# Kernel tuning notes

Measured on AMD Instinct MI355X. Metric: run time of the kernel, lower is better.

## Reference

```python
import jax, jax.numpy as jnp
import numpy as np

NUM_NODES = 20000
SEQ_LEN = 128
IN_FEATS = 2
HIDDEN = 32
N_TOTAL = NUM_NODES * SEQ_LEN  # flattened graph size
N_EDGES = 2_000_000


def setup_inputs() -> dict:
    key = jax.random.key(0)
    ks = jax.random.split(key, 10)
    x = jax.random.normal(ks[0], (NUM_NODES, SEQ_LEN, IN_FEATS), dtype=jnp.float32)
    edge_index = jax.random.randint(ks[1], (2, N_EDGES), 0, N_TOTAL, dtype=jnp.int64)
    s = 0.1
    gcn_W = jax.random.normal(ks[2], (IN_FEATS, HIDDEN), dtype=jnp.float32) * s
    gcn_b = jnp.zeros((HIDDEN,), dtype=jnp.float32)
    w_ih = jax.random.normal(ks[3], (4 * HIDDEN, HIDDEN), dtype=jnp.float32) * s
    w_hh = jax.random.normal(ks[4], (4 * HIDDEN, HIDDEN), dtype=jnp.float32) * s
    b_ih = jax.random.normal(ks[5], (4 * HIDDEN,), dtype=jnp.float32) * s
    b_hh = jax.random.normal(ks[6], (4 * HIDDEN,), dtype=jnp.float32) * s
    fc_W = jax.random.normal(ks[7], (HIDDEN, 1), dtype=jnp.float32) * s
    fc_b = jnp.zeros((1,), dtype=jnp.float32)
    return {"x": x, "edge_index": edge_index, "gcn_W": gcn_W, "gcn_b": gcn_b,
            "w_ih": w_ih, "w_hh": w_hh, "b_ih": b_ih, "b_hh": b_hh,
            "fc_W": fc_W, "fc_b": fc_b}


def _gcn(x_flat, edge_index, W, b):
    # PyG GCNConv: add self-loops, symmetric normalization, then linear+bias.
    src, dst = edge_index[0], edge_index[1]
    n = x_flat.shape[0]
    # degree at target side, including the self-loop (+1)
    deg = jax.ops.segment_sum(jnp.ones_like(dst, dtype=x_flat.dtype), dst, num_segments=n) + 1.0
    dinv = jax.lax.rsqrt(deg)  # deg >= 1 always (self-loop)
    h = x_flat @ W  # [n, HIDDEN] transform before propagate
    norm = dinv[src] * dinv[dst]  # [E]
    msg = h[src] * norm[:, None]  # gather + per-edge scale
    agg = jax.ops.segment_sum(msg, dst, num_segments=n)
    # self-loop contribution: dinv_i * dinv_i * h_i = h_i / deg_i
    out = agg + h * (1.0 / deg)[:, None]
    return out + b


def _lstm(xs, w_ih, w_hh, b_ih, b_hh):
    # torch LSTM gate order: i, f, g, o. xs: [N, S, H] -> final hidden [N, H]
    n, s, hdim = xs.shape
    xs_t = jnp.swapaxes(xs, 0, 1)  # [S, N, H]
    # precompute input projections once (dense GEMM)
    x_proj = xs_t @ w_ih.T + b_ih + b_hh  # [S, N, 4H]

    def step(carry, xp):
        h, c = carry
        g = xp + h @ w_hh.T  # [N, 4H]
        i, f, gg, o = jnp.split(g, 4, axis=-1)
        c = jax.nn.sigmoid(f) * c + jax.nn.sigmoid(i) * jnp.tanh(gg)
        h = jax.nn.sigmoid(o) * jnp.tanh(c)
        return (h, c), None

    h0 = jnp.zeros((n, hdim), dtype=xs.dtype)
    (hn, _), _ = jax.lax.scan(step, (h0, h0), x_proj)
    return hn


def reference(x, edge_index, gcn_W, gcn_b, w_ih, w_hh, b_ih, b_hh, fc_W, fc_b):
    num_nodes, seq_len, num_feats = x.shape
    x_in = x.reshape(-1, num_feats)  # [N*S, F]
    x_gcn = jax.nn.relu(_gcn(x_in, edge_index, gcn_W, gcn_b))
    x_lstm = x_gcn.reshape(num_nodes, seq_len, -1)
    hn = _lstm(x_lstm, w_ih, w_hh, b_ih, b_hh)
    return hn @ fc_W + fc_b  # [num_nodes, 1]
```

## Files before the change

### kernel.cpp

```cpp
#include <hip/hip_runtime.h>

#define SEQ 128
#define HID 32
#define TPB 128
#define XS 56

typedef __attribute__((ext_vector_type(8))) short short8;
typedef __attribute__((ext_vector_type(4))) short short4v;
typedef __attribute__((ext_vector_type(4))) float floatx4;


__global__ void count_kernel(const int* __restrict__ idx, int E, int* __restrict__ cnt) {
    int e = (blockIdx.x * blockDim.x + threadIdx.x) * 4;
    if (((E & 3) == 0) && e + 3 < E) {
        int4 d = *(const int4*)(idx + E + e);
        atomicAdd(&cnt[d.x], 1);
        atomicAdd(&cnt[d.y], 1);
        atomicAdd(&cnt[d.z], 1);
        atomicAdd(&cnt[d.w], 1);
    } else {
        int lim = min(e + 4, E);
        for (int k = e; k < lim; ++k) atomicAdd(&cnt[idx[E + k]], 1);
    }
}

__global__ void dinv_xs_pk_kernel(const int* __restrict__ deg, float* __restrict__ dinv,
                                  const float2* __restrict__ x2, float2* __restrict__ xs2,
                                  int n) {
    int i = blockIdx.x * blockDim.x + threadIdx.x;
    if (i < n) {
        float dv = rsqrtf((float)deg[i] + 1.0f);
        dinv[i] = dv;
        float2 xx = x2[i];
        xs2[i] = make_float2(xx.x * dv, xx.y * dv);
    }
}

__global__ void dinv_kernel(float* __restrict__ buf, int n) {
    int i = blockIdx.x * blockDim.x + threadIdx.x;
    if (i < n) buf[i] = rsqrtf((float)__float_as_int(buf[i]) + 1.0f);
}

__device__ __forceinline__ unsigned long long pk2(float2 v) {
    int qx = __float2int_rn(v.x * 2097152.0f);
    int qy = __float2int_rn(v.y * 2097152.0f);
    return ((unsigned long long)(unsigned)(qx + (1 << 26)) << 32) |
           (unsigned)(qy + (1 << 26));
}

__global__ void scatter_pk_kernel(const int* __restrict__ idx, int E,
                                  const float2* __restrict__ xs2,
                                  unsigned long long* __restrict__ aggP) {
    int e = (blockIdx.x * blockDim.x + threadIdx.x) * 4;
    if (((E & 3) == 0) && e + 3 < E) {
        int4 s = *(const int4*)(idx + e);
        int4 d = *(const int4*)(idx + E + e);
        float2 v0 = xs2[s.x];
        float2 v1 = xs2[s.y];
        float2 v2 = xs2[s.z];
        float2 v3 = xs2[s.w];
        atomicAdd(&aggP[d.x], pk2(v0));
        atomicAdd(&aggP[d.y], pk2(v1));
        atomicAdd(&aggP[d.z], pk2(v2));
        atomicAdd(&aggP[d.w], pk2(v3));
    } else {
        int lim = min(e + 4, E);
        for (int k = e; k < lim; ++k) {
            int s = idx[k];
            int d = idx[E + k];
            atomicAdd(&aggP[d], pk2(xs2[s]));
        }
    }
}

__global__ void scatter_kernel(const int* __restrict__ idx, int E,
                               const float2* __restrict__ x2,
                               const float* __restrict__ dinv,
                               float* __restrict__ agg2) {
    int e = blockIdx.x * blockDim.x + threadIdx.x;
    if (e < E) {
        int s = idx[e];
        int d = idx[E + e];
        float ns = dinv[s];
        float2 xs = x2[s];
        unsafeAtomicAdd(&agg2[2 * d + 0], xs.x * ns);
        unsafeAtomicAdd(&agg2[2 * d + 1], xs.y * ns);
    }
}


__device__ __forceinline__ float sigm_f(float x) {
    return __builtin_amdgcn_rcpf(1.0f + __expf(-x));
}
__device__ __forceinline__ float tanh_f(float x) {
    return fmaf(__builtin_amdgcn_rcpf(1.0f + __expf(-2.0f * x)), 2.0f, -1.0f);
}
__device__ __forceinline__ void fsplit(float f, short& hi, short& lo) {
    unsigned u = __float_as_uint(f);
    hi = (short)(u >> 16);
    float r = f - __uint_as_float(u & 0xFFFF0000u);
    lo = (short)(__float_as_uint(r) >> 16);
}

__global__ __launch_bounds__(TPB, 2) void lstm_mfma3_kernel(
    const float2* __restrict__ x2, const float* __restrict__ dinv,
    const float2* __restrict__ agg2,
    const unsigned long long* __restrict__ aggP, const int* __restrict__ deg,
    int packed, int N,
    const float* __restrict__ gcn_W, const float* __restrict__ gcn_b,
    const float* __restrict__ w_ih, const float* __restrict__ w_hh,
    const float* __restrict__ b_ih, const float* __restrict__ b_hh,
    const float* __restrict__ fc_W, const float* __restrict__ fc_b,
    float* __restrict__ out) {
    __shared__ float2 ubuf[16][SEQ + 1];
    __shared__ __align__(16) short xgh[2][16][XS];
    __shared__ __align__(16) short xgl[2][16][XS];
    __shared__ __align__(16) short hhb[2][16][XS];
    __shared__ __align__(16) short hlb[2][16][XS];
    __shared__ float fcp[2][16];

    const int tid = threadIdx.x;
    const int w = tid >> 6;
    const int lane = tid & 63;
    const int l15 = lane & 15;
    const int q = lane >> 4;
    const int base = blockIdx.x * 16;

    {
        const float2* xb  = x2   + (size_t)base * SEQ;
        const float*  db  = dinv + (size_t)base * SEQ;
        const float2* agb = agg2 + (size_t)base * SEQ;
        const unsigned long long* apb = aggP + (size_t)base * SEQ;
        const int* dgb = deg + (size_t)base * SEQ;
        const int lim = min(16 * SEQ, (N - base) * SEQ);
        for (int i = tid; i < 16 * SEQ; i += TPB) {
            float2 v = make_float2(0.f, 0.f);
            if (i < lim) {
                float dv = db[i];
                float2 xx = xb[i];
                float ax, ay;
                if (packed) {
                    unsigned long long pk = apb[i];
                    unsigned bias = (unsigned)dgb[i] * 67108864u;
                    ax = (float)((int)((unsigned)(pk >> 32) - bias)) * (1.0f / 2097152.0f);
                    ay = (float)((int)((unsigned)pk - bias)) * (1.0f / 2097152.0f);
                } else {
                    float2 a = agb[i];
                    ax = a.x; ay = a.y;
                }
                v = make_float2(dv * fmaf(xx.x, dv, ax), dv * fmaf(xx.y, dv, ay));
            }
            ubuf[i >> 7][i & 127] = v;
        }
    }

    short8 AiH[4], AiL[4], AhH[4], AhL[4];
    floatx4 biasC[4];
    #pragma unroll
    for (int g = 0; g < 4; ++g) {
        const int arow = g * 32 + 8 * (l15 >> 2) + 4 * w + (l15 & 3);
        const float* wi = w_ih + arow * HID + 8 * q;
        const float* wh = w_hh + arow * HID + 8 * q;
        #pragma unroll
        for (int j = 0; j < 8; ++j) {
            short h16, l16;
            fsplit(wi[j], h16, l16); AiH[g][j] = h16; AiL[g][j] = l16;
            fsplit(wh[j], h16, l16); AhH[g][j] = h16; AhL[g][j] = l16;
        }
        #pragma unroll
        for (int r = 0; r < 4; ++r) {
            const int brow = g * 32 + 8 * q + 4 * w + r;
            biasC[g][r] = b_ih[brow] + b_hh[brow];
        }
    }

    float wg0[4], wg1[4], gbc[4], fcw[4];
    #pragma unroll
    for (int r = 0; r < 4; ++r) {
        const int u = 16 * w + 4 * q + r;
        wg0[r] = gcn_W[u];
        wg1[r] = gcn_W[HID + u];
        gbc[r] = gcn_b[u];
        fcw[r] = fc_W[8 * q + 4 * w + r];
    }

    float c[4] = {0.f, 0.f, 0.f, 0.f};
    float ho[4] = {0.f, 0.f, 0.f, 0.f};

    __syncthreads();

    {
        float2 uu = ubuf[l15][0];
        short hi[4], lo[4];
        #pragma unroll
        for (int r = 0; r < 4; ++r) {
            float g = fmaxf(fmaf(uu.x, wg0[r], fmaf(uu.y, wg1[r], gbc[r])), 0.f);
            fsplit(g, hi[r], lo[r]);
        }
        *(short4v*)&xgh[0][l15][16 * w + 4 * q] = (short4v){hi[0], hi[1], hi[2], hi[3]};
        *(short4v*)&xgl[0][l15][16 * w + 4 * q] = (short4v){lo[0], lo[1], lo[2], lo[3]};
        *(short4v*)&hhb[0][l15][8 * q + 4 * w] = (short4v){0, 0, 0, 0};
        *(short4v*)&hlb[0][l15][8 * q + 4 * w] = (short4v){0, 0, 0, 0};
    }
    __syncthreads();

#define LSTM_STEP(P, TT)                                                                   \
    do {                                                                                   \
        const short8 xh = *(const short8*)&xgh[P][l15][8 * q];                             \
        const short8 xl = *(const short8*)&xgl[P][l15][8 * q];                             \
        const short8 hh = *(const short8*)&hhb[P][l15][8 * q];                             \
        const short8 hl = *(const short8*)&hlb[P][l15][8 * q];                             \
        floatx4 acc[4];                                                                    \
        __builtin_amdgcn_s_setprio(1);                                                     \
        _Pragma("unroll") for (int g = 0; g < 4; ++g)                                      \
            acc[g] = __builtin_amdgcn_mfma_f32_16x16x32_bf16(AiH[g], xh, biasC[g], 0, 0, 0); \
        _Pragma("unroll") for (int g = 0; g < 4; ++g)                                      \
            acc[g] = __builtin_amdgcn_mfma_f32_16x16x32_bf16(AiL[g], xh, acc[g], 0, 0, 0); \
        _Pragma("unroll") for (int g = 0; g < 4; ++g)                                      \
            acc[g] = __builtin_amdgcn_mfma_f32_16x16x32_bf16(AiH[g], xl, acc[g], 0, 0, 0); \
        _Pragma("unroll") for (int g = 0; g < 4; ++g)                                      \
            acc[g] = __builtin_amdgcn_mfma_f32_16x16x32_bf16(AhH[g], hh, acc[g], 0, 0, 0); \
        _Pragma("unroll") for (int g = 0; g < 4; ++g)                                      \
            acc[g] = __builtin_amdgcn_mfma_f32_16x16x32_bf16(AhL[g], hh, acc[g], 0, 0, 0); \
        _Pragma("unroll") for (int g = 0; g < 4; ++g)                                      \
            acc[g] = __builtin_amdgcn_mfma_f32_16x16x32_bf16(AhH[g], hl, acc[g], 0, 0, 0); \
        __builtin_amdgcn_s_setprio(0);                                                     \
        {                                                                                  \
            float2 uu = ubuf[l15][(TT) + 1];          \
            short hi[4], lo[4];                                                            \
            _Pragma("unroll") for (int r = 0; r < 4; ++r) {                                \
                float g = fmaxf(fmaf(uu.x, wg0[r], fmaf(uu.y, wg1[r], gbc[r])), 0.f);      \
                fsplit(g, hi[r], lo[r]);                                                   \
            }                                                                              \
            *(short4v*)&xgh[(P) ^ 1][l15][16 * w + 4 * q] =                                \
                (short4v){hi[0], hi[1], hi[2], hi[3]};                                     \
            *(short4v*)&xgl[(P) ^ 1][l15][16 * w + 4 * q] =                                \
                (short4v){lo[0], lo[1], lo[2], lo[3]};                                     \
        }                                                                                  \
        {                                                                                  \
            short hi[4], lo[4];                                                            \
            _Pragma("unroll") for (int r = 0; r < 4; ++r) {                                \
                const float ig = sigm_f(acc[0][r]);                                        \
                const float fg = sigm_f(acc[1][r]);                                        \
                const float gg = tanh_f(acc[2][r]);                                        \
                const float og = sigm_f(acc[3][r]);                                        \
                c[r] = fmaf(fg, c[r], ig * gg);                                            \
                const float hv = og * tanh_f(c[r]);                                        \
                ho[r] = hv;                                                                \
                fsplit(hv, hi[r], lo[r]);                                                  \
            }                                                                              \
            *(short4v*)&hhb[(P) ^ 1][l15][8 * q + 4 * w] =                                 \
                (short4v){hi[0], hi[1], hi[2], hi[3]};                                     \
            *(short4v*)&hlb[(P) ^ 1][l15][8 * q + 4 * w] =                                 \
                (short4v){lo[0], lo[1], lo[2], lo[3]};                                     \
        }                                                                                  \
        __syncthreads();                                                                   \
    } while (0)

    #pragma unroll 1
    for (int t = 0; t < SEQ; t += 2) {
        LSTM_STEP(0, t);
        LSTM_STEP(1, t + 1);
    }
#undef LSTM_STEP

    float partial = fmaf(ho[0], fcw[0], fmaf(ho[1], fcw[1],
                    fmaf(ho[2], fcw[2], ho[3] * fcw[3])));
    partial += __shfl_xor(partial, 16);
    partial += __shfl_xor(partial, 32);
    if (lane < 16) fcp[w][l15] = partial;
    __syncthreads();
    if (w == 0 && lane < 16) {
        const int node = base + l15;
        if (node < N) out[node] = fcp[0][l15] + fcp[1][l15] + fc_b[0];
    }
}

extern "C" void kernel_launch(void* const* d_in, const int* in_sizes, int n_in,
                              void* d_out, int out_size, void* d_ws, size_t ws_size,
                              hipStream_t stream) {
    const float* x     = (const float*)d_in[0];
    const int*   idx   = (const int*)d_in[1];
    const float* gcn_W = (const float*)d_in[2];
    const float* gcn_b = (const float*)d_in[3];
    const float* w_ih  = (const float*)d_in[4];
    const float* w_hh  = (const float*)d_in[5];
    const float* b_ih  = (const float*)d_in[6];
    const float* b_hh  = (const float*)d_in[7];
    const float* fc_W  = (const float*)d_in[8];
    const float* fc_b  = (const float*)d_in[9];

    const int num_nodes = in_sizes[0] / (SEQ * 2);
    const int ntot = num_nodes * SEQ;
    const int E = in_sizes[1] / 2;

    float* dinv = (float*)d_ws;
    int* deg = (int*)d_ws + ntot;
    unsigned long long* aggP = (unsigned long long*)((float*)d_ws + 2 * (size_t)ntot);
    float* xs2 = (float*)d_ws + 4 * (size_t)ntot;
    const bool packed = ws_size >= (size_t)ntot * sizeof(float) * 6;

    const int eb = (E + 1023) / 1024;
    if (packed) {
        hipMemsetAsync(deg, 0, (size_t)ntot * sizeof(float) * 3, stream);
        count_kernel<<<eb, 256, 0, stream>>>(idx, E, deg);
        dinv_xs_pk_kernel<<<(ntot + 255) / 256, 256, 0, stream>>>(
            deg, dinv, (const float2*)x, (float2*)xs2, ntot);
        scatter_pk_kernel<<<eb, 256, 0, stream>>>(idx, E, (const float2*)xs2, aggP);
        lstm_mfma3_kernel<<<(num_nodes + 15) / 16, TPB, 0, stream>>>(
            (const float2*)x, dinv, (const float2*)xs2 , aggP, deg, 1, num_nodes,
            gcn_W, gcn_b, w_ih, w_hh, b_ih, b_hh, fc_W, fc_b, (float*)d_out);
    } else {
        float* agg2 = (float*)d_ws + ntot;
        hipMemsetAsync(d_ws, 0, (size_t)ntot * sizeof(float) * 3, stream);
        count_kernel<<<eb, 256, 0, stream>>>(idx, E, (int*)dinv);
        dinv_kernel<<<(ntot + 255) / 256, 256, 0, stream>>>(dinv, ntot);
        scatter_kernel<<<(E + 255) / 256, 256, 0, stream>>>(
            idx, E, (const float2*)x, dinv, agg2);
        lstm_mfma3_kernel<<<(num_nodes + 15) / 16, TPB, 0, stream>>>(
            (const float2*)x, dinv, (const float2*)agg2,
            (const unsigned long long*)agg2 , (const int*)dinv ,
            0, num_nodes,
            gcn_W, gcn_b, w_ih, w_hh, b_ih, b_hh, fc_W, fc_b, (float*)d_out);
    }
}
```

Measured before the change: 476.2 us.

## Fold dinv kernel into scatter and LSTM, compute input-gate frags in registers

Removes the separate dinv/xs pre-scale kernel: the scatter now gathers x and deg per source edge and computes rsqrt inline, and the LSTM kernel recomputes dinv from deg. Inside the LSTM, the GCN-output fragments are built directly in registers as MFMA B operands, and the input-projection MFMAs for step t+1 are issued during step t instead of going through LDS xgh/xgl buffers. The unpacked fallback path is dropped. This trades one pass over memory and some LDS traffic for extra random gathers of deg in the scatter and higher register pressure.

```diff
diff --git a/kernel.cpp b/kernel.cpp
--- a/kernel.cpp
+++ b/kernel.cpp
@@ -24,67 +24,42 @@
     }
 }
 
-__global__ void dinv_xs_pk_kernel(const int* __restrict__ deg, float* __restrict__ dinv,
-                                  const float2* __restrict__ x2, float2* __restrict__ xs2,
-                                  int n) {
-    int i = blockIdx.x * blockDim.x + threadIdx.x;
-    if (i < n) {
-        float dv = rsqrtf((float)deg[i] + 1.0f);
-        dinv[i] = dv;
-        float2 xx = x2[i];
-        xs2[i] = make_float2(xx.x * dv, xx.y * dv);
-    }
-}
-
-__global__ void dinv_kernel(float* __restrict__ buf, int n) {
-    int i = blockIdx.x * blockDim.x + threadIdx.x;
-    if (i < n) buf[i] = rsqrtf((float)__float_as_int(buf[i]) + 1.0f);
-}
-
-__device__ __forceinline__ unsigned long long pk2(float2 v) {
-    int qx = __float2int_rn(v.x * 2097152.0f);
-    int qy = __float2int_rn(v.y * 2097152.0f);
+__device__ __forceinline__ unsigned long long pk2(float xx, float yy, float dv) {
+    int qx = __float2int_rn(xx * dv * 2097152.0f);
+    int qy = __float2int_rn(yy * dv * 2097152.0f);
     return ((unsigned long long)(unsigned)(qx + (1 << 26)) << 32) |
            (unsigned)(qy + (1 << 26));
 }
 
 __global__ void scatter_pk_kernel(const int* __restrict__ idx, int E,
-                                  const float2* __restrict__ xs2,
+                                  const float2* __restrict__ x2,
+                                  const int* __restrict__ deg,
                                   unsigned long long* __restrict__ aggP) {
     int e = (blockIdx.x * blockDim.x + threadIdx.x) * 4;
     if (((E & 3) == 0) && e + 3 < E) {
         int4 s = *(const int4*)(idx + e);
         int4 d = *(const int4*)(idx + E + e);
-        float2 v0 = xs2[s.x];
-        float2 v1 = xs2[s.y];
-        float2 v2 = xs2[s.z];
-        float2 v3 = xs2[s.w];
-        atomicAdd(&aggP[d.x], pk2(v0));
-        atomicAdd(&aggP[d.y], pk2(v1));
-        atomicAdd(&aggP[d.z], pk2(v2));
-        atomicAdd(&aggP[d.w], pk2(v3));
+        float2 v0 = x2[s.x];
+        float2 v1 = x2[s.y];
+        float2 v2 = x2[s.z];
+        float2 v3 = x2[s.w];
+        float dv0 = rsqrtf((float)deg[s.x] + 1.0f);
+        float dv1 = rsqrtf((float)deg[s.y] + 1.0f);
+        float dv2 = rsqrtf((float)deg[s.z] + 1.0f);
+        float dv3 = rsqrtf((float)deg[s.w] + 1.0f);
+        atomicAdd(&aggP[d.x], pk2(v0.x, v0.y, dv0));
+        atomicAdd(&aggP[d.y], pk2(v1.x, v1.y, dv1));
+        atomicAdd(&aggP[d.z], pk2(v2.x, v2.y, dv2));
+        atomicAdd(&aggP[d.w], pk2(v3.x, v3.y, dv3));
     } else {
         int lim = min(e + 4, E);
         for (int k = e; k < lim; ++k) {
             int s = idx[k];
             int d = idx[E + k];
-            atomicAdd(&aggP[d], pk2(xs2[s]));
-        }
-    }
-}
-
-__global__ void scatter_kernel(const int* __restrict__ idx, int E,
-                               const float2* __restrict__ x2,
-                               const float* __restrict__ dinv,
-                               float* __restrict__ agg2) {
-    int e = blockIdx.x * blockDim.x + threadIdx.x;
-    if (e < E) {
-        int s = idx[e];
-        int d = idx[E + e];
-        float ns = dinv[s];
-        float2 xs = x2[s];
-        unsafeAtomicAdd(&agg2[2 * d + 0], xs.x * ns);
-        unsafeAtomicAdd(&agg2[2 * d + 1], xs.y * ns);
+            float2 v = x2[s];
+            float dv = rsqrtf((float)deg[s] + 1.0f);
+            atomicAdd(&aggP[d], pk2(v.x, v.y, dv));
+        }
     }
 }
 
@@ -102,19 +77,16 @@
     lo = (short)(__float_as_uint(r) >> 16);
 }
 
-__global__ __launch_bounds__(TPB, 2) void lstm_mfma3_kernel(
-    const float2* __restrict__ x2, const float* __restrict__ dinv,
-    const float2* __restrict__ agg2,
+__global__ __launch_bounds__(TPB, 2) void lstm_mfma4_kernel(
+    const float2* __restrict__ x2,
     const unsigned long long* __restrict__ aggP, const int* __restrict__ deg,
-    int packed, int N,
+    int N,
     const float* __restrict__ gcn_W, const float* __restrict__ gcn_b,
     const float* __restrict__ w_ih, const float* __restrict__ w_hh,
     const float* __restrict__ b_ih, const float* __restrict__ b_hh,
     const float* __restrict__ fc_W, const float* __restrict__ fc_b,
     float* __restrict__ out) {
     __shared__ float2 ubuf[16][SEQ + 1];
-    __shared__ __align__(16) short xgh[2][16][XS];
-    __shared__ __align__(16) short xgl[2][16][XS];
     __shared__ __align__(16) short hhb[2][16][XS];
     __shared__ __align__(16) short hlb[2][16][XS];
     __shared__ float fcp[2][16];
@@ -127,31 +99,25 @@
     const int base = blockIdx.x * 16;
 
     {
-        const float2* xb  = x2   + (size_t)base * SEQ;
-        const float*  db  = dinv + (size_t)base * SEQ;
-        const float2* agb = agg2 + (size_t)base * SEQ;
+        const float2* xb = x2 + (size_t)base * SEQ;
         const unsigned long long* apb = aggP + (size_t)base * SEQ;
         const int* dgb = deg + (size_t)base * SEQ;
         const int lim = min(16 * SEQ, (N - base) * SEQ);
         for (int i = tid; i < 16 * SEQ; i += TPB) {
             float2 v = make_float2(0.f, 0.f);
             if (i < lim) {
-                float dv = db[i];
+                int dg = dgb[i];
+                float dv = rsqrtf((float)dg + 1.0f);
                 float2 xx = xb[i];
-                float ax, ay;
-                if (packed) {
-                    unsigned long long pk = apb[i];
-                    unsigned bias = (unsigned)dgb[i] * 67108864u;
-                    ax = (float)((int)((unsigned)(pk >> 32) - bias)) * (1.0f / 2097152.0f);
-                    ay = (float)((int)((unsigned)pk - bias)) * (1.0f / 2097152.0f);
-                } else {
-                    float2 a = agb[i];
-                    ax = a.x; ay = a.y;
-                }
+                unsigned long long pk = apb[i];
+                unsigned bias = (unsigned)dg * 67108864u;
+                float ax = (float)((int)((unsigned)(pk >> 32) - bias)) * (1.0f / 2097152.0f);
+                float ay = (float)((int)((unsigned)pk - bias)) * (1.0f / 2097152.0f);
                 v = make_float2(dv * fmaf(xx.x, dv, ax), dv * fmaf(xx.y, dv, ay));
             }
             ubuf[i >> 7][i & 127] = v;
         }
+        if (tid < 16) ubuf[tid][SEQ] = make_float2(0.f, 0.f);
     }
 
     short8 AiH[4], AiL[4], AhH[4], AhL[4];
@@ -174,69 +140,72 @@
         }
     }
 
-    float wg0[4], wg1[4], gbc[4], fcw[4];
-    #pragma unroll
-    for (int r = 0; r < 4; ++r) {
-        const int u = 16 * w + 4 * q + r;
-        wg0[r] = gcn_W[u];
-        wg1[r] = gcn_W[HID + u];
-        gbc[r] = gcn_b[u];
-        fcw[r] = fc_W[8 * q + 4 * w + r];
-    }
+    float wg0[8], wg1[8], gbc[8];
+    #pragma unroll
+    for (int j = 0; j < 8; ++j) {
+        const int u = 8 * q + j;
+        wg0[j] = gcn_W[u];
+        wg1[j] = gcn_W[HID + u];
+        gbc[j] = gcn_b[u];
+    }
+    float fcw[4];
+    #pragma unroll
+    for (int r = 0; r < 4; ++r) fcw[r] = fc_W[8 * q + 4 * w + r];
 
     float c[4] = {0.f, 0.f, 0.f, 0.f};
     float ho[4] = {0.f, 0.f, 0.f, 0.f};
 
     __syncthreads();
 
-    {
-        float2 uu = ubuf[l15][0];
-        short hi[4], lo[4];
-        #pragma unroll
-        for (int r = 0; r < 4; ++r) {
-            float g = fmaxf(fmaf(uu.x, wg0[r], fmaf(uu.y, wg1[r], gbc[r])), 0.f);
-            fsplit(g, hi[r], lo[r]);
-        }
-        *(short4v*)&xgh[0][l15][16 * w + 4 * q] = (short4v){hi[0], hi[1], hi[2], hi[3]};
-        *(short4v*)&xgl[0][l15][16 * w + 4 * q] = (short4v){lo[0], lo[1], lo[2], lo[3]};
-        *(short4v*)&hhb[0][l15][8 * q + 4 * w] = (short4v){0, 0, 0, 0};
-        *(short4v*)&hlb[0][l15][8 * q + 4 * w] = (short4v){0, 0, 0, 0};
-    }
+#define XG_FRAGS(TT, XH, XL)                                                  \
+    {                                                                         \
+        float2 uu = ubuf[l15][TT];                                            \
+        _Pragma("unroll") for (int j = 0; j < 8; ++j) {                       \
+            float g = fmaxf(fmaf(uu.x, wg0[j], fmaf(uu.y, wg1[j], gbc[j])), 0.f); \
+            short h16, l16;                                                   \
+            fsplit(g, h16, l16);                                              \
+            XH[j] = h16; XL[j] = l16;                                         \
+        }                                                                     \
+    }
+
+    *(short4v*)&hhb[0][l15][8 * q + 4 * w] = (short4v){0, 0, 0, 0};
+    *(short4v*)&hlb[0][l15][8 * q + 4 * w] = (short4v){0, 0, 0, 0};
+    short8 xhA, xlA, xhB, xlB;
+    floatx4 aXA[4], aXB[4];
+    XG_FRAGS(0, xhA, xlA);
+    #pragma unroll
+    for (int g = 0; g < 4; ++g)
+        aXA[g] = __builtin_amdgcn_mfma_f32_16x16x32_bf16(AiH[g], xhA, biasC[g], 0, 0, 0);
+    #pragma unroll
+    for (int g = 0; g < 4; ++g)
+        aXA[g] = __builtin_amdgcn_mfma_f32_16x16x32_bf16(AiL[g], xhA, aXA[g], 0, 0, 0);
+    #pragma unroll
+    for (int g = 0; g < 4; ++g)
+        aXA[g] = __builtin_amdgcn_mfma_f32_16x16x32_bf16(AiH[g], xlA, aXA[g], 0, 0, 0);
     __syncthreads();
 
-#define LSTM_STEP(P, TT)                                                                   \
+#define LSTM_STEP(P, TT, AXC, AXN, XHN, XLN)                                               \
     do {                                                                                   \
-        const short8 xh = *(const short8*)&xgh[P][l15][8 * q];                             \
-        const short8 xl = *(const short8*)&xgl[P][l15][8 * q];                             \
         const short8 hh = *(const short8*)&hhb[P][l15][8 * q];                             \
         const short8 hl = *(const short8*)&hlb[P][l15][8 * q];                             \
         floatx4 acc[4];                                                                    \
         __builtin_amdgcn_s_setprio(1);                                                     \
         _Pragma("unroll") for (int g = 0; g < 4; ++g)                                      \
-            acc[g] = __builtin_amdgcn_mfma_f32_16x16x32_bf16(AiH[g], xh, biasC[g], 0, 0, 0); \
-        _Pragma("unroll") for (int g = 0; g < 4; ++g)                                      \
-            acc[g] = __builtin_amdgcn_mfma_f32_16x16x32_bf16(AiL[g], xh, acc[g], 0, 0, 0); \
-        _Pragma("unroll") for (int g = 0; g < 4; ++g)                                      \
-            acc[g] = __builtin_amdgcn_mfma_f32_16x16x32_bf16(AiH[g], xl, acc[g], 0, 0, 0); \
-        _Pragma("unroll") for (int g = 0; g < 4; ++g)                                      \
-            acc[g] = __builtin_amdgcn_mfma_f32_16x16x32_bf16(AhH[g], hh, acc[g], 0, 0, 0); \
+            acc[g] = __builtin_amdgcn_mfma_f32_16x16x32_bf16(AhH[g], hh, AXC[g], 0, 0, 0); \
         _Pragma("unroll") for (int g = 0; g < 4; ++g)                                      \
             acc[g] = __builtin_amdgcn_mfma_f32_16x16x32_bf16(AhL[g], hh, acc[g], 0, 0, 0); \
         _Pragma("unroll") for (int g = 0; g < 4; ++g)                                      \
             acc[g] = __builtin_amdgcn_mfma_f32_16x16x32_bf16(AhH[g], hl, acc[g], 0, 0, 0); \
         __builtin_amdgcn_s_setprio(0);                                                     \
-        {                                                                                  \
-            float2 uu = ubuf[l15][(TT) + 1];          \
-            short hi[4], lo[4];                                                            \
-            _Pragma("unroll") for (int r = 0; r < 4; ++r) {                                \
-                float g = fmaxf(fmaf(uu.x, wg0[r], fmaf(uu.y, wg1[r], gbc[r])), 0.f);      \
-                fsplit(g, hi[r], lo[r]);                                                   \
-            }                                                                              \
-            *(short4v*)&xgh[(P) ^ 1][l15][16 * w + 4 * q] =                                \
-                (short4v){hi[0], hi[1], hi[2], hi[3]};                                     \
-            *(short4v*)&xgl[(P) ^ 1][l15][16 * w + 4 * q] =                                \
-                (short4v){lo[0], lo[1], lo[2], lo[3]};                                     \
-        }                                                                                  \
+        XG_FRAGS((TT) + 1, XHN, XLN);                                                      \
+        __builtin_amdgcn_s_setprio(1);                                                     \
+        _Pragma("unroll") for (int g = 0; g < 4; ++g)                                      \
+            AXN[g] = __builtin_amdgcn_mfma_f32_16x16x32_bf16(AiH[g], XHN, biasC[g], 0, 0, 0); \
+        _Pragma("unroll") for (int g = 0; g < 4; ++g)                                      \
+            AXN[g] = __builtin_amdgcn_mfma_f32_16x16x32_bf16(AiL[g], XHN, AXN[g], 0, 0, 0); \
+        _Pragma("unroll") for (int g = 0; g < 4; ++g)                                      \
+            AXN[g] = __builtin_amdgcn_mfma_f32_16x16x32_bf16(AiH[g], XLN, AXN[g], 0, 0, 0); \
+        __builtin_amdgcn_s_setprio(0);                                                     \
         {                                                                                  \
             short hi[4], lo[4];                                                            \
             _Pragma("unroll") for (int r = 0; r < 4; ++r) {                                \
@@ -259,10 +228,11 @@
 
     #pragma unroll 1
     for (int t = 0; t < SEQ; t += 2) {
-        LSTM_STEP(0, t);
-        LSTM_STEP(1, t + 1);
+        LSTM_STEP(0, t,     aXA, aXB, xhB, xlB);
+        LSTM_STEP(1, t + 1, aXB, aXA, xhA, xlA);
     }
 #undef LSTM_STEP
+#undef XG_FRAGS
 
     float partial = fmaf(ho[0], fcw[0], fmaf(ho[1], fcw[1],
                     fmaf(ho[2], fcw[2], ho[3] * fcw[3])));
@@ -294,33 +264,16 @@
     const int ntot = num_nodes * SEQ;
     const int E = in_sizes[1] / 2;
 
-    float* dinv = (float*)d_ws;
-    int* deg = (int*)d_ws + ntot;
-    unsigned long long* aggP = (unsigned long long*)((float*)d_ws + 2 * (size_t)ntot);
-    float* xs2 = (float*)d_ws + 4 * (size_t)ntot;
-    const bool packed = ws_size >= (size_t)ntot * sizeof(float) * 6;
+    int* deg = (int*)d_ws;
+    unsigned long long* aggP = (unsigned long long*)((char*)d_ws + (size_t)ntot * 4);
+
+    hipMemsetAsync(d_ws, 0, (size_t)ntot * 12, stream);
 
     const int eb = (E + 1023) / 1024;
-    if (packed) {
-        hipMemsetAsync(deg, 0, (size_t)ntot * sizeof(float) * 3, stream);
-        count_kernel<<<eb, 256, 0, stream>>>(idx, E, deg);
-        dinv_xs_pk_kernel<<<(ntot + 255) / 256, 256, 0, stream>>>(
-            deg, dinv, (const float2*)x, (float2*)xs2, ntot);
-        scatter_pk_kernel<<<eb, 256, 0, stream>>>(idx, E, (const float2*)xs2, aggP);
-        lstm_mfma3_kernel<<<(num_nodes + 15) / 16, TPB, 0, stream>>>(
-            (const float2*)x, dinv, (const float2*)xs2 , aggP, deg, 1, num_nodes,
-            gcn_W, gcn_b, w_ih, w_hh, b_ih, b_hh, fc_W, fc_b, (float*)d_out);
-    } else {
-        float* agg2 = (float*)d_ws + ntot;
-        hipMemsetAsync(d_ws, 0, (size_t)ntot * sizeof(float) * 3, stream);
-        count_kernel<<<eb, 256, 0, stream>>>(idx, E, (int*)dinv);
-        dinv_kernel<<<(ntot + 255) / 256, 256, 0, stream>>>(dinv, ntot);
-        scatter_kernel<<<(E + 255) / 256, 256, 0, stream>>>(
-            idx, E, (const float2*)x, dinv, agg2);
-        lstm_mfma3_kernel<<<(num_nodes + 15) / 16, TPB, 0, stream>>>(
-            (const float2*)x, dinv, (const float2*)agg2,
-            (const unsigned long long*)agg2 , (const int*)dinv ,
-            0, num_nodes,
-            gcn_W, gcn_b, w_ih, w_hh, b_ih, b_hh, fc_W, fc_b, (float*)d_out);
-    }
-}
+    count_kernel<<<eb, 256, 0, stream>>>(idx, E, deg);
+    scatter_pk_kernel<<<eb, 256, 0, stream>>>(idx, E, (const float2*)x, deg, aggP);
+    lstm_mfma4_kernel<<<(num_nodes + 15) / 16, TPB, 0, stream>>>(
+        (const float2*)x, aggP, deg, num_nodes,
+        gcn_W, gcn_b, w_ih, w_hh, b_ih, b_hh, fc_W, fc_b,
+        (float*)d_out);
+}
```

Result: slower. 489.5 us (+2.8%).
